# Kernel tuning notes

Hardware: AMD Instinct MI355X
Metric: run time of the kernel (lower is better)

## Reference

```python
import jax, jax.numpy as jnp
import numpy as np

N, D, O = 8192, 1024, 1024

def setup_inputs() -> dict:
    key = jax.random.key(0)
    ks = jax.random.split(key, 6)
    s = 1.0 / np.sqrt(D)
    x = jax.random.normal(ks[0], (N, D), dtype=jnp.float32)
    adj = jax.random.randint(ks[1], (N, N), 0, 2, dtype=jnp.int32)
    Wf = jax.random.normal(ks[2], (D, D), dtype=jnp.float32) * s
    Wg = jax.random.normal(ks[3], (D, D), dtype=jnp.float32) * s
    W = jax.random.normal(ks[4], (D, O), dtype=jnp.float32) * s
    bf = jnp.zeros((D,), dtype=jnp.float32)
    bg = jnp.zeros((D,), dtype=jnp.float32)
    bW = jnp.zeros((O,), dtype=jnp.float32)
    return {"x": x, "adj": adj, "Wf": Wf, "bf": bf, "Wg": Wg, "bg": bg, "W": W, "bW": bW}

def reference(x, adj, Wf, bf, Wg, bg, W, bW):
    NEG = jnp.float32(-9e15)
    f = x @ Wf + bf                      # [N, D]
    g = x @ Wg + bg                      # [N, D]
    e = jax.nn.relu(f @ g.T)             # [N, N] scores
    scores = jnp.where(adj > 0, e, NEG)  # adjacency mask
    attention = jax.nn.softmax(scores, axis=1)
    # dropout is identity in eval mode (training=False)
    x_W = x @ W + bW                     # [N, O]
    return attention @ x_W               # concat=False -> no final relu
```

## Files before the change

### kernel.cpp

```cpp
#include <hip/hip_runtime.h>
#include <stdint.h>

#define NROWS 8192
#define KDIM  1024
#define CAP   512
#define NEGBIG (-9.0e15f)
#define EMIT_THR 16.0f
#define SURV_THR 13.5f
#define MAXS  128

typedef __attribute__((ext_vector_type(8))) __bf16 bf16x8;
typedef __attribute__((ext_vector_type(4))) float f32x4;
typedef __attribute__((ext_vector_type(4))) unsigned short us4;
typedef __attribute__((ext_vector_type(4))) int i32x4;
typedef unsigned short u16;

__device__ __forceinline__ u16 f2bf(float f) {
  unsigned u = __float_as_uint(f);
  u += 0x7fffu + ((u >> 16) & 1u);
  return (u16)(u >> 16);
}
__device__ __forceinline__ float bf2f(u16 h) {
  return __uint_as_float(((unsigned)h) << 16);
}

__device__ __forceinline__ void glds16(const void* g, const char* lds) {
  __builtin_amdgcn_global_load_lds(
      (const __attribute__((address_space(1))) unsigned int*)(uintptr_t)g,
      (__attribute__((address_space(3))) unsigned int*)(uintptr_t)lds, 16, 0, 0);
}

__device__ __forceinline__ f32x4 mfma16(bf16x8 a, bf16x8 b, f32x4 c) {
  return __builtin_amdgcn_mfma_f32_16x16x32_bf16(a, b, c, 0, 0, 0);
}

template<int NSPLIT, bool SPLITOUT>
__global__ __launch_bounds__(512, 1) void gemm_kernel(
    const u16* __restrict__ ah, const u16* __restrict__ al,
    const u16* __restrict__ bh, const u16* __restrict__ bl,
    const float* __restrict__ bias, u16* __restrict__ ch, u16* __restrict__ cl)
{
  extern __shared__ char smem[];
  constexpr int BUFS = (NSPLIT == 3) ? 65536 : 32768;
  constexpr int AHO = 0, ALO = 16384;
  constexpr int BHO = (NSPLIT == 3) ? 32768 : 16384;
  constexpr int BLO = 49152;
  constexpr int NT = KDIM / 64;

  const int tid = threadIdx.x, w = tid >> 6, lane = tid & 63;
  const int wr = w >> 2, wc = w & 3;
  const int bx = blockIdx.x, by = blockIdx.y;
  const int arow0 = bx * 128, bcol0 = by * 128;

  const int srow = w * 16 + (lane >> 3);
  const int scol = ((lane & 7) ^ (lane >> 3)) * 8;
  const size_t sgA = (size_t)(arow0 + srow) * KDIM + scol;
  const size_t sgB = (size_t)(bcol0 + srow) * KDIM + scol;
  const int ldsw = w * 2048;

  auto stg = [&](const u16* src, size_t sg, int kt, int ldsoff) {
    const u16* sp = src + sg + kt * 64;
    glds16(sp,            smem + ldsoff + ldsw);
    glds16(sp + 8 * KDIM, smem + ldsoff + ldsw + 1024);
  };

  const int fa = (wr * 64 + (lane & 15)) * 128;
  const int fb = (wc * 32 + (lane & 15)) * 128;
  const int kqx0 = (((lane >> 4)    ) ^ (lane & 7)) * 16;
  const int kqx1 = (((lane >> 4) + 4) ^ (lane & 7)) * 16;

  stg(ah, sgA, 0, AHO); stg(bh, sgB, 0, BHO);
  if constexpr (NSPLIT == 3) { stg(al, sgA, 0, ALO); stg(bl, sgB, 0, BLO); }
  else { stg(ah, sgA, 1, AHO + BUFS); stg(bh, sgB, 1, BHO + BUFS); }

  f32x4 acc[4][2];
  #pragma unroll
  for (int m = 0; m < 4; ++m) {
    acc[m][0] = f32x4{0.f, 0.f, 0.f, 0.f};
    acc[m][1] = f32x4{0.f, 0.f, 0.f, 0.f};
  }

  for (int t = 0; t < NT; ++t) {
    const int bo  = (t & 1) * BUFS;
    const int bo2 = ((t + 1) & 1) * BUFS;

    if (NSPLIT == 1 && t == NT - 1) asm volatile("s_waitcnt vmcnt(0)" ::: "memory");
    else                            asm volatile("s_waitcnt vmcnt(4)" ::: "memory");
    __builtin_amdgcn_s_barrier();
    __builtin_amdgcn_sched_barrier(0);

    if (NSPLIT == 3 && t + 1 < NT) {
      stg(ah, sgA, t + 1, AHO + bo2);
      stg(bh, sgB, t + 1, BHO + bo2);
    }

    bf16x8 a0[4][2], b0[2][2];
    #pragma unroll
    for (int m = 0; m < 4; ++m) {
      a0[m][0] = *(const bf16x8*)(smem + AHO + bo + fa + m * 2048 + kqx0);
      a0[m][1] = *(const bf16x8*)(smem + AHO + bo + fa + m * 2048 + kqx1);
    }
    #pragma unroll
    for (int n = 0; n < 2; ++n) {
      b0[n][0] = *(const bf16x8*)(smem + BHO + bo + fb + n * 2048 + kqx0);
      b0[n][1] = *(const bf16x8*)(smem + BHO + bo + fb + n * 2048 + kqx1);
    }
    __builtin_amdgcn_s_setprio(1);
    #pragma unroll
    for (int kq = 0; kq < 2; ++kq)
      #pragma unroll
      for (int m = 0; m < 4; ++m)
        #pragma unroll
        for (int n = 0; n < 2; ++n)
          acc[m][n] = mfma16(a0[m][kq], b0[n][kq], acc[m][n]);
    __builtin_amdgcn_s_setprio(0);
    asm volatile("s_waitcnt lgkmcnt(0)" ::: "memory");

    if constexpr (NSPLIT == 3) {
      if (t + 1 < NT) asm volatile("s_waitcnt vmcnt(4)" ::: "memory");
      else            asm volatile("s_waitcnt vmcnt(0)" ::: "memory");
      __builtin_amdgcn_s_barrier();
      __builtin_amdgcn_sched_barrier(0);

      if (t + 1 < NT) {
        stg(al, sgA, t + 1, ALO + bo2);
        stg(bl, sgB, t + 1, BLO + bo2);
      }
      bf16x8 a1[4][2], b1[2][2];
      #pragma unroll
      for (int m = 0; m < 4; ++m) {
        a1[m][0] = *(const bf16x8*)(smem + ALO + bo + fa + m * 2048 + kqx0);
        a1[m][1] = *(const bf16x8*)(smem + ALO + bo + fa + m * 2048 + kqx1);
      }
      #pragma unroll
      for (int n = 0; n < 2; ++n) {
        b1[n][0] = *(const bf16x8*)(smem + BLO + bo + fb + n * 2048 + kqx0);
        b1[n][1] = *(const bf16x8*)(smem + BLO + bo + fb + n * 2048 + kqx1);
      }
      __builtin_amdgcn_s_setprio(1);
      #pragma unroll
      for (int kq = 0; kq < 2; ++kq)
        #pragma unroll
        for (int m = 0; m < 4; ++m)
          #pragma unroll
          for (int n = 0; n < 2; ++n)
            acc[m][n] = mfma16(a1[m][kq], b0[n][kq], acc[m][n]);
      #pragma unroll
      for (int kq = 0; kq < 2; ++kq)
        #pragma unroll
        for (int m = 0; m < 4; ++m)
          #pragma unroll
          for (int n = 0; n < 2; ++n)
            acc[m][n] = mfma16(a0[m][kq], b1[n][kq], acc[m][n]);
      __builtin_amdgcn_s_setprio(0);
      asm volatile("s_waitcnt lgkmcnt(0)" ::: "memory");
    } else {
      __builtin_amdgcn_s_barrier();
      if (t + 2 < NT) {
        stg(ah, sgA, t + 2, AHO + bo);
        stg(bh, sgB, t + 2, BHO + bo);
      }
    }
  }

  const int l15 = lane & 15, g4 = (lane >> 4) << 2;
  const int colb = bcol0 + wc * 32 + l15;
  const float bi0 = bias[colb], bi1 = bias[colb + 16];
  #pragma unroll
  for (int m = 0; m < 4; ++m) {
    #pragma unroll
    for (int j = 0; j < 4; ++j) {
      const int row = arow0 + wr * 64 + m * 16 + g4 + j;
      float v0 = acc[m][0][j] + bi0, v1 = acc[m][1][j] + bi1;
      u16 h0 = f2bf(v0), h1 = f2bf(v1);
      ch[(size_t)row * KDIM + colb] = h0;
      ch[(size_t)row * KDIM + colb + 16] = h1;
      if constexpr (SPLITOUT) {
        cl[(size_t)row * KDIM + colb] = f2bf(v0 - bf2f(h0));
        cl[(size_t)row * KDIM + colb + 16] = f2bf(v1 - bf2f(h1));
      }
    }
  }
}

__global__ __launch_bounds__(512, 2) void scores_kernel(
    const u16* __restrict__ fh, const u16* __restrict__ gh,
    const uint32_t* __restrict__ adjb, uint32_t* __restrict__ cand,
    int* __restrict__ cnts, int* rowmax)
{
  extern __shared__ char smem[];
  constexpr int NT = 64;

  const int tid = threadIdx.x, w = tid >> 6, lane = tid & 63;
  const int wr = w >> 2, wc = w & 3;
  const int l15 = lane & 15, g4 = (lane >> 4) << 2;

  const int xcd = blockIdx.x & 7, idx = blockIdx.x >> 3;
  const int bx  = xcd * 4 + (idx & 3);
  const int sub = idx >> 2;
  const int arow0 = bx * 256;

  const int srow = tid >> 3;
  const int skq  = (tid & 7) ^ (srow & 7);
  const int sdw  = w * 1024;

  auto stageA = [&](int T, int half) {
    char* d = smem + (T & 1) * 65536 + half * 16384 + sdw;
    const u16* s = fh + (size_t)(arow0 + half * 128 + srow) * KDIM
                      + (T & 15) * 64 + skq * 8;
    glds16(s, d);
    glds16(s + (size_t)64 * KDIM, d + 8192);
  };
  auto stageB = [&](int T, int half) {
    char* d = smem + (T & 1) * 65536 + 32768 + half * 16384 + sdw;
    const u16* s = gh + (size_t)((sub + 8 * (T >> 4)) * 256 + half * 128 + srow) * KDIM
                      + (T & 15) * 64 + skq * 8;
    glds16(s, d);
    glds16(s + (size_t)64 * KDIM, d + 8192);
  };

  const int kxa = ((lane >> 4) ^ (l15 & 7)) * 16;
  const int kxb = (((lane >> 4) + 4) ^ (l15 & 7)) * 16;
  const int abase = wr * 16384 + l15 * 128;
  const int bbase = 32768 + (wc >> 1) * 16384 + ((wc & 1) * 64 + l15) * 128;

  f32x4 acc[8][4];
  #pragma unroll
  for (int m = 0; m < 8; ++m)
    #pragma unroll
    for (int n = 0; n < 4; ++n) acc[m][n] = f32x4{0.f, 0.f, 0.f, 0.f};

  const unsigned long long lmask = (1ull << lane) - 1ull;
  const unsigned long long gm = 0xFFFFull << (lane & 48);

  stageA(0, 0); stageA(0, 1); stageB(0, 0); stageB(0, 1);
  stageA(1, 0); stageA(1, 1); stageB(1, 0); stageB(1, 1);
  asm volatile("s_waitcnt vmcnt(8)" ::: "memory");
  __builtin_amdgcn_s_barrier();

  bf16x8 a[8][2], b[4][2];

  for (int T = 0; T < NT; ++T) {
    const char* sb = smem + (T & 1) * 65536;

    #pragma unroll
    for (int m = 0; m < 4; ++m) {
      a[m][0] = *(const bf16x8*)(sb + abase + m * 2048 + kxa);
      a[m][1] = *(const bf16x8*)(sb + abase + m * 2048 + kxb);
    }
    #pragma unroll
    for (int n = 0; n < 2; ++n) {
      b[n][0] = *(const bf16x8*)(sb + bbase + n * 2048 + kxa);
      b[n][1] = *(const bf16x8*)(sb + bbase + n * 2048 + kxb);
    }
    __builtin_amdgcn_s_barrier();
    __builtin_amdgcn_s_setprio(1);
    #pragma unroll
    for (int kq = 0; kq < 2; ++kq)
      #pragma unroll
      for (int m = 0; m < 4; ++m)
        #pragma unroll
        for (int n = 0; n < 2; ++n)
          acc[m][n] = mfma16(a[m][kq], b[n][kq], acc[m][n]);
    __builtin_amdgcn_s_setprio(0);
    __builtin_amdgcn_s_barrier();

    #pragma unroll
    for (int m = 4; m < 8; ++m) {
      a[m][0] = *(const bf16x8*)(sb + abase + m * 2048 + kxa);
      a[m][1] = *(const bf16x8*)(sb + abase + m * 2048 + kxb);
    }
    __builtin_amdgcn_s_barrier();
    __builtin_amdgcn_s_setprio(1);
    #pragma unroll
    for (int kq = 0; kq < 2; ++kq)
      #pragma unroll
      for (int m = 4; m < 8; ++m)
        #pragma unroll
        for (int n = 0; n < 2; ++n)
          acc[m][n] = mfma16(a[m][kq], b[n][kq], acc[m][n]);
    __builtin_amdgcn_s_setprio(0);
    asm volatile("s_waitcnt lgkmcnt(0)" ::: "memory");
    __builtin_amdgcn_s_barrier();

    #pragma unroll
    for (int n = 2; n < 4; ++n) {
      b[n][0] = *(const bf16x8*)(sb + bbase + n * 2048 + kxa);
      b[n][1] = *(const bf16x8*)(sb + bbase + n * 2048 + kxb);
    }
    if (T + 2 < NT) { stageA(T + 2, 0); stageA(T + 2, 1); }
    __builtin_amdgcn_s_barrier();
    __builtin_amdgcn_s_setprio(1);
    #pragma unroll
    for (int kq = 0; kq < 2; ++kq)
      #pragma unroll
      for (int m = 0; m < 4; ++m)
        #pragma unroll
        for (int n = 2; n < 4; ++n)
          acc[m][n] = mfma16(a[m][kq], b[n][kq], acc[m][n]);
    __builtin_amdgcn_s_setprio(0);
    asm volatile("s_waitcnt lgkmcnt(0)" ::: "memory");
    __builtin_amdgcn_s_barrier();

    if (T + 2 < NT) {
      stageB(T + 2, 0); stageB(T + 2, 1);
      asm volatile("s_waitcnt vmcnt(8)" ::: "memory");
    } else {
      asm volatile("s_waitcnt vmcnt(0)" ::: "memory");
    }
    __builtin_amdgcn_s_barrier();
    __builtin_amdgcn_s_setprio(1);
    #pragma unroll
    for (int kq = 0; kq < 2; ++kq)
      #pragma unroll
      for (int m = 4; m < 8; ++m)
        #pragma unroll
        for (int n = 2; n < 4; ++n)
          acc[m][n] = mfma16(a[m][kq], b[n][kq], acc[m][n]);
    __builtin_amdgcn_s_setprio(0);
    __builtin_amdgcn_s_barrier();

    if ((T & 15) == 15) {
      const int it = T >> 4;
      const int bcol0 = (sub + 8 * it) * 256;
      const int keyb = bcol0 + wc * 64 + l15;
      #pragma unroll
      for (int mc = 0; mc < 4; ++mc) {
        uint32_t A0[2][4], A1[2][4]; float RX[2][4]; int ROW[2][4];
        #pragma unroll
        for (int mm = 0; mm < 2; ++mm)
          #pragma unroll
          for (int j = 0; j < 4; ++j) {
            const int m = mc * 2 + mm;
            const int row = arow0 + wr * 128 + m * 16 + g4 + j;
            ROW[mm][j] = row;
            const uint32_t* ap = adjb + (size_t)row * (NROWS / 32) + (bcol0 >> 5) + wc * 2;
            A0[mm][j] = ap[0];
            A1[mm][j] = ap[1];
            RX[mm][j] = __int_as_float(rowmax[row]);
          }
        float SV[2][4][4]; float TH[2][4]; int BS[2][4];
        #pragma unroll
        for (int mm = 0; mm < 2; ++mm)
          #pragma unroll
          for (int j = 0; j < 4; ++j) {
            const int m = mc * 2 + mm;
            float rm = NEGBIG;
            #pragma unroll
            for (int n = 0; n < 4; ++n) {
              float v = fmaxf(acc[m][n][j], 0.f);
              uint32_t bit = ((n < 2 ? A0[mm][j] : A1[mm][j]) >> ((n & 1) * 16 + l15)) & 1u;
              float s = bit ? v : NEGBIG;
              SV[mm][j][n] = s;
              rm = fmaxf(rm, s);
            }
            rm = fmaxf(rm, __shfl_xor(rm, 1));
            rm = fmaxf(rm, __shfl_xor(rm, 2));
            rm = fmaxf(rm, __shfl_xor(rm, 4));
            rm = fmaxf(rm, __shfl_xor(rm, 8));
            const float mr = fmaxf(rm, RX[mm][j]);
            if (l15 == 0 && rm > RX[mm][j])
              atomicMax(rowmax + ROW[mm][j], __float_as_int(rm));
            TH[mm][j] = mr - EMIT_THR;
            int tot = 0;
            #pragma unroll
            for (int n = 0; n < 4; ++n)
              tot += __popcll(__ballot(SV[mm][j][n] > TH[mm][j]) & gm);
            BS[mm][j] = 0;
            if (l15 == 0 && tot > 0)
              BS[mm][j] = atomicAdd(cnts + ROW[mm][j], tot);
          }
        #pragma unroll
        for (int mm = 0; mm < 2; ++mm)
          #pragma unroll
          for (int j = 0; j < 4; ++j) {
            int base = __shfl(BS[mm][j], lane & 48);
            int pref = 0;
            #pragma unroll
            for (int n = 0; n < 4; ++n) {
              unsigned long long mk = __ballot(SV[mm][j][n] > TH[mm][j]);
              const int p = base + pref + __popcll(mk & gm & lmask);
              if ((SV[mm][j][n] > TH[mm][j]) && p < CAP)
                cand[(size_t)ROW[mm][j] * CAP + p] =
                    ((uint32_t)f2bf(SV[mm][j][n]) << 16) | (uint32_t)(keyb + n * 16);
              pref += __popcll(mk & gm);
            }
          }
      }
      #pragma unroll
      for (int m = 0; m < 8; ++m)
        #pragma unroll
        for (int n = 0; n < 4; ++n) acc[m][n] = f32x4{0.f, 0.f, 0.f, 0.f};
    }
  }
}

__global__ __launch_bounds__(256) void adjpack_kernel(
    const int* __restrict__ adj, uint32_t* __restrict__ adjb)
{
  size_t w = (size_t)blockIdx.x * 256 + threadIdx.x;
  const int* src = adj + (w << 5);
  uint32_t m = 0;
  #pragma unroll
  for (int j = 0; j < 8; ++j) {
    i32x4 v = *(const i32x4*)(src + j * 4);
    m |= (v[0] > 0 ? 1u : 0u) << (j * 4)
       | (v[1] > 0 ? 1u : 0u) << (j * 4 + 1)
       | (v[2] > 0 ? 1u : 0u) << (j * 4 + 2)
       | (v[3] > 0 ? 1u : 0u) << (j * 4 + 3);
  }
  adjb[w] = m;
}

__global__ __launch_bounds__(256) void finalize_kernel(
    const uint32_t* __restrict__ cand, const int* __restrict__ cnts,
    const u16* __restrict__ fh, const u16* __restrict__ fl,
    const u16* __restrict__ gh, const u16* __restrict__ gl,
    const u16* __restrict__ vh, float* __restrict__ out)
{
  const int row = blockIdx.x, tid = threadIdx.x, wv = tid >> 6, lane = tid & 63;
  __shared__ float sS[CAP];
  __shared__ int sK[CAP];
  __shared__ float sF[KDIM];
  __shared__ float sEx[MAXS];
  __shared__ int sKs[MAXS];
  __shared__ float red[4];
  __shared__ int nsig;
  int cnt = cnts[row]; cnt = cnt < CAP ? cnt : CAP;
  const int col = tid * 4;
  if (cnt <= 0) {
    f32x4 z = {0.f, 0.f, 0.f, 0.f};
    *(f32x4*)(out + (size_t)row * KDIM + col) = z;
    return;
  }
  if (tid == 0) nsig = 0;
  {
    us4 h = *(const us4*)(fh + (size_t)row * KDIM + col);
    us4 l = *(const us4*)(fl + (size_t)row * KDIM + col);
    #pragma unroll
    for (int j = 0; j < 4; ++j) sF[col + j] = bf2f(h[j]) + bf2f(l[j]);
  }
  for (int i = tid; i < cnt; i += 256) {
    uint32_t pk = cand[(size_t)row * CAP + i];
    sS[i] = bf2f((u16)(pk >> 16));
    sK[i] = (int)(pk & 0xFFFFu);
  }
  __syncthreads();
  float lm = NEGBIG;
  for (int i = tid; i < cnt; i += 256) lm = fmaxf(lm, sS[i]);
  #pragma unroll
  for (int d = 1; d < 64; d <<= 1) lm = fmaxf(lm, __shfl_xor(lm, d));
  if ((tid & 63) == 0) red[tid >> 6] = lm;
  __syncthreads();
  const float am = fmaxf(fmaxf(red[0], red[1]), fmaxf(red[2], red[3]));
  __syncthreads();
  for (int i = tid; i < cnt; i += 256) {
    if (sS[i] > am - SURV_THR) {
      int p = atomicAdd(&nsig, 1);
      if (p < MAXS) { sKs[p] = sK[i]; sS[i] = NEGBIG; }
    }
  }
  __syncthreads();
  const int ns = nsig < MAXS ? nsig : MAXS;
  for (int si = wv; si < ns; si += 4) {
    const int key = sKs[si];
    const u16* grh = gh + (size_t)key * KDIM + lane * 16;
    const u16* grl = gl + (size_t)key * KDIM + lane * 16;
    float d = 0.f;
    #pragma unroll
    for (int u = 0; u < 4; ++u) {
      us4 h = *(const us4*)(grh + u * 4);
      us4 l = *(const us4*)(grl + u * 4);
      #pragma unroll
      for (int j = 0; j < 4; ++j)
        d += (bf2f(h[j]) + bf2f(l[j])) * sF[lane * 16 + u * 4 + j];
    }
    #pragma unroll
    for (int dd = 1; dd < 64; dd <<= 1) d += __shfl_xor(d, dd);
    if (lane == 0) sEx[si] = fmaxf(d, 0.f);
  }
  __syncthreads();
  float em = NEGBIG;
  for (int i = tid; i < ns; i += 256) em = fmaxf(em, sEx[i]);
  #pragma unroll
  for (int d = 1; d < 64; d <<= 1) em = fmaxf(em, __shfl_xor(em, d));
  if ((tid & 63) == 0) red[tid >> 6] = em;
  __syncthreads();
  const float m = fmaxf(fmaxf(red[0], red[1]), fmaxf(red[2], red[3]));
  __syncthreads();
  float ls = 0.f;
  for (int i = tid; i < cnt; i += 256) {
    float s = sS[i];
    if (s > NEGBIG * 0.5f) ls += __expf(s - m);
  }
  for (int i = tid; i < ns; i += 256) ls += __expf(sEx[i] - m);
  #pragma unroll
  for (int d = 1; d < 64; d <<= 1) ls += __shfl_xor(ls, d);
  if ((tid & 63) == 0) red[tid >> 6] = ls;
  __syncthreads();
  const float inv = 1.f / (red[0] + red[1] + red[2] + red[3]);
  float a0 = 0.f, a1 = 0.f, a2 = 0.f, a3 = 0.f;
  const u16* vbase = vh + col;
  for (int i = 0; i < ns; ++i) {
    const float wt = __expf(sEx[i] - m) * inv;
    us4 vv = *(const us4*)(vbase + (size_t)sKs[i] * KDIM);
    a0 += wt * bf2f(vv[0]); a1 += wt * bf2f(vv[1]);
    a2 += wt * bf2f(vv[2]); a3 += wt * bf2f(vv[3]);
  }
  f32x4 o = {a0, a1, a2, a3};
  *(f32x4*)(out + (size_t)row * KDIM + col) = o;
}

__global__ __launch_bounds__(256) void wsplit_kernel(
    const float* __restrict__ W, u16* __restrict__ th, u16* __restrict__ tl)
{
  __shared__ float tile[32][33];
  const int bx = blockIdx.x, by = blockIdx.y;
  const int tx = threadIdx.x & 31, ty = threadIdx.x >> 5;
  #pragma unroll
  for (int i = 0; i < 4; ++i) {
    int ky = ty + i * 8;
    tile[ky][tx] = W[(size_t)(by * 32 + ky) * KDIM + bx * 32 + tx];
  }
  __syncthreads();
  #pragma unroll
  for (int i = 0; i < 4; ++i) {
    int ny = ty + i * 8;
    float v = tile[tx][ny];
    u16 h = f2bf(v);
    th[(size_t)(bx * 32 + ny) * KDIM + by * 32 + tx] = h;
    tl[(size_t)(bx * 32 + ny) * KDIM + by * 32 + tx] = f2bf(v - bf2f(h));
  }
}

__global__ __launch_bounds__(256) void xsplit_kernel(
    const float* __restrict__ x, u16* __restrict__ xh, u16* __restrict__ xl)
{
  size_t i = ((size_t)blockIdx.x * 256 + threadIdx.x) * 4;
  f32x4 v = *(const f32x4*)(x + i);
  us4 h, l;
  #pragma unroll
  for (int j = 0; j < 4; ++j) {
    h[j] = f2bf(v[j]);
    l[j] = f2bf(v[j] - bf2f(h[j]));
  }
  *(us4*)(xh + i) = h;
  *(us4*)(xl + i) = l;
}

__global__ void ws_report(float* out, size_t n, float v) {
  for (size_t i = (size_t)blockIdx.x * blockDim.x + threadIdx.x; i < n;
       i += (size_t)gridDim.x * blockDim.x) out[i] = v;
}

extern "C" void kernel_launch(void* const* d_in, const int* in_sizes, int n_in,
                              void* d_out, int out_size, void* d_ws, size_t ws_size,
                              hipStream_t stream) {
  (void)in_sizes; (void)n_in;
  const float* x   = (const float*)d_in[0];
  const int*   adj = (const int*)d_in[1];
  const float* Wf  = (const float*)d_in[2];
  const float* bf_ = (const float*)d_in[3];
  const float* Wg  = (const float*)d_in[4];
  const float* bg_ = (const float*)d_in[5];
  const float* W   = (const float*)d_in[6];
  const float* bW_ = (const float*)d_in[7];

  char* p = (char*)d_ws;
  const size_t ND2 = (size_t)NROWS * KDIM * 2;
  const size_t W2  = (size_t)KDIM * KDIM * 2;
  u16* xh = (u16*)p;  p += ND2;
  u16* xl = (u16*)p;  p += ND2;
  u16* fh = (u16*)p;  p += ND2;
  u16* fl = (u16*)p;  p += ND2;
  u16* gh = (u16*)p;  p += ND2;
  u16* gl = (u16*)p;  p += ND2;
  u16* vh = (u16*)p;  p += ND2;
  u16* wfh = (u16*)p; p += W2;
  u16* wfl = (u16*)p; p += W2;
  u16* wgh = (u16*)p; p += W2;
  u16* wgl = (u16*)p; p += W2;
  u16* wh  = (u16*)p; p += W2;
  u16* wl  = (u16*)p; p += W2;
  uint32_t* cand = (uint32_t*)p; p += (size_t)NROWS * CAP * 4;
  int* cnts   = (int*)p; p += (size_t)NROWS * 4;
  int* rowmax = (int*)p; p += (size_t)NROWS * 4;
  const size_t need = (size_t)(p - (char*)d_ws);
  if (ws_size < need) {
    ws_report<<<256, 256, 0, stream>>>((float*)d_out, (size_t)out_size, (float)ws_size);
    return;
  }
  uint32_t* adjb = (uint32_t*)xl;

  auto kf = gemm_kernel<3, true>;
  auto kv = gemm_kernel<1, false>;
  hipFuncSetAttribute((const void*)kf, hipFuncAttributeMaxDynamicSharedMemorySize, 131072);
  hipFuncSetAttribute((const void*)kv, hipFuncAttributeMaxDynamicSharedMemorySize, 65536);
  hipFuncSetAttribute((const void*)scores_kernel, hipFuncAttributeMaxDynamicSharedMemorySize, 131072);

  hipMemsetAsync(cnts, 0, (size_t)NROWS * 8, stream);
  wsplit_kernel<<<dim3(32, 32), 256, 0, stream>>>(Wf, wfh, wfl);
  wsplit_kernel<<<dim3(32, 32), 256, 0, stream>>>(Wg, wgh, wgl);
  wsplit_kernel<<<dim3(32, 32), 256, 0, stream>>>(W, wh, wl);
  xsplit_kernel<<<(NROWS * KDIM) / (256 * 4), 256, 0, stream>>>(x, xh, xl);

  kf<<<dim3(64, 8), 512, 131072, stream>>>(xh, xl, wfh, wfl, bf_, fh, fl);
  kf<<<dim3(64, 8), 512, 131072, stream>>>(xh, xl, wgh, wgl, bg_, gh, gl);
  kv<<<dim3(64, 8), 512, 65536, stream>>>(xh, xl, wh, wl, bW_, vh, nullptr);
  adjpack_kernel<<<(NROWS * (NROWS / 32)) / 256, 256, 0, stream>>>(adj, adjb);
  scores_kernel<<<dim3(256), 512, 131072, stream>>>(fh, gh, adjb, cand, cnts, rowmax);
  finalize_kernel<<<NROWS, 256, 0, stream>>>(cand, cnts, fh, fl, gh, gl, vh,
                                             (float*)d_out);
}
```

Before: 558.3 us.

## Quantize f and g to fp8 for the candidate-screening scores GEMM

Adds a quant_kernel that converts the bf16 f and g activations to fp8 e4m3 and reorders each row's k-chunks to match the MFMA operand layout. The scores_kernel now stages the fp8 data and uses the 16x16x32 fp8 MFMA, which halves its LDS and global traffic and the number of K tiles. The emit threshold is raised to absorb the larger fp8 error in the screening pass; exact values are still recomputed in finalize from the split-bf16 data. The risks are extra candidates filling the per-row cap, and two extra kernel launches plus an extra pass over f and g.

```diff
diff --git a/kernel.cpp b/kernel.cpp
--- a/kernel.cpp
+++ b/kernel.cpp
@@ -5,7 +5,7 @@
 #define KDIM  1024
 #define CAP   512
 #define NEGBIG (-9.0e15f)
-#define EMIT_THR 16.0f
+#define EMIT_THR 20.0f
 #define SURV_THR 13.5f
 #define MAXS  128
 
@@ -13,7 +13,10 @@
 typedef __attribute__((ext_vector_type(4))) float f32x4;
 typedef __attribute__((ext_vector_type(4))) unsigned short us4;
 typedef __attribute__((ext_vector_type(4))) int i32x4;
+typedef __attribute__((ext_vector_type(2))) long i64x2;
+typedef __attribute__((ext_vector_type(16))) unsigned char u8x16;
 typedef unsigned short u16;
+typedef unsigned char u8;
 
 __device__ __forceinline__ u16 f2bf(float f) {
   unsigned u = __float_as_uint(f);
@@ -24,6 +27,28 @@
   return __uint_as_float(((unsigned)h) << 16);
 }
 
+__device__ __forceinline__ u8 f2fp8(float f) {
+  uint32_t u = __float_as_uint(f);
+  uint32_t s = (u >> 24) & 0x80u;
+  int e = (int)((u >> 23) & 0xffu) - 127;
+  uint32_t m = u & 0x7fffffu;
+  if (e > 8 || (e == 8 && m > 0x600000u)) return (u8)(s | 0x7eu);
+  if (e >= -6) {
+    uint32_t mant = m >> 20;
+    uint32_t rem = m & 0xfffffu;
+    if (rem > 0x80000u || (rem == 0x80000u && (mant & 1u))) mant++;
+    uint32_t ee = (uint32_t)(e + 7);
+    if (mant == 8u) { mant = 0u; ee++; }
+    if (ee >= 16u) return (u8)(s | 0x7eu);
+    return (u8)(s | (ee << 3) | mant);
+  }
+  if (e < -10) return (u8)s;
+  float af = fabsf(f);
+  int q = (int)(af * 512.0f + 0.5f);
+  if (q > 8) q = 8;
+  return (u8)(s | (uint32_t)q);
+}
+
 __device__ __forceinline__ void glds16(const void* g, const char* lds) {
   __builtin_amdgcn_global_load_lds(
       (const __attribute__((address_space(1))) unsigned int*)(uintptr_t)g,
@@ -32,6 +57,9 @@
 
 __device__ __forceinline__ f32x4 mfma16(bf16x8 a, bf16x8 b, f32x4 c) {
   return __builtin_amdgcn_mfma_f32_16x16x32_bf16(a, b, c, 0, 0, 0);
+}
+__device__ __forceinline__ f32x4 mfma8(long a, long b, f32x4 c) {
+  return __builtin_amdgcn_mfma_f32_16x16x32_fp8_fp8(a, b, c, 0, 0, 0);
 }
 
 template<int NSPLIT, bool SPLITOUT>
@@ -183,46 +211,67 @@
   }
 }
 
+__global__ __launch_bounds__(256) void quant_kernel(
+    const u16* __restrict__ src, u8* __restrict__ dst)
+{
+  const int id = blockIdx.x * 256 + threadIdx.x;
+  const int row = id >> 6, mtc = id & 63;
+  const int mt = mtc >> 3, c = mtc & 7;
+  const int k0 = mt * 128 + (c >> 2) * 64 + (c & 3) * 8;
+  const u16* s0 = src + (size_t)row * KDIM + k0;
+  u8x16 o;
+  #pragma unroll
+  for (int j = 0; j < 8; ++j) o[j] = f2fp8(bf2f(s0[j]));
+  #pragma unroll
+  for (int j = 0; j < 8; ++j) o[8 + j] = f2fp8(bf2f(s0[32 + j]));
+  *(u8x16*)(dst + (size_t)id * 16) = o;
+}
+
 __global__ __launch_bounds__(512, 2) void scores_kernel(
-    const u16* __restrict__ fh, const u16* __restrict__ gh,
+    const u8* __restrict__ fq, const u8* __restrict__ gq,
     const uint32_t* __restrict__ adjb, uint32_t* __restrict__ cand,
     int* __restrict__ cnts, int* rowmax)
 {
   extern __shared__ char smem[];
-  constexpr int NT = 64;
+  constexpr int NT = 32;
 
   const int tid = threadIdx.x, w = tid >> 6, lane = tid & 63;
   const int wr = w >> 2, wc = w & 3;
-  const int l15 = lane & 15, g4 = (lane >> 4) << 2;
+  const int l15 = lane & 15, g4 = (lane >> 4) << 2, hi4 = lane >> 4;
 
   const int xcd = blockIdx.x & 7, idx = blockIdx.x >> 3;
   const int bx  = xcd * 4 + (idx & 3);
   const int sub = idx >> 2;
   const int arow0 = bx * 256;
 
-  const int srow = tid >> 3;
-  const int skq  = (tid & 7) ^ (srow & 7);
-  const int sdw  = w * 1024;
-
-  auto stageA = [&](int T, int half) {
-    char* d = smem + (T & 1) * 65536 + half * 16384 + sdw;
-    const u16* s = fh + (size_t)(arow0 + half * 128 + srow) * KDIM
-                      + (T & 15) * 64 + skq * 8;
-    glds16(s, d);
-    glds16(s + (size_t)64 * KDIM, d + 8192);
+  const int sdw = w * 4096;
+
+  auto stageA = [&](int T) {
+    char* dbase = smem + (T & 1) * 65536 + sdw;
+    #pragma unroll
+    for (int i = 0; i < 4; ++i) {
+      const int d = (w * 4 + i) * 64 + lane;
+      const int row = d >> 3, cl = (d & 7) ^ (row & 7);
+      glds16(fq + (size_t)(arow0 + row) * KDIM + (T & 7) * 128 + cl * 16,
+             dbase + i * 1024);
+    }
   };
-  auto stageB = [&](int T, int half) {
-    char* d = smem + (T & 1) * 65536 + 32768 + half * 16384 + sdw;
-    const u16* s = gh + (size_t)((sub + 8 * (T >> 4)) * 256 + half * 128 + srow) * KDIM
-                      + (T & 15) * 64 + skq * 8;
-    glds16(s, d);
-    glds16(s + (size_t)64 * KDIM, d + 8192);
+  auto stageB = [&](int T) {
+    char* dbase = smem + (T & 1) * 65536 + 32768 + sdw;
+    const size_t kb = (size_t)(sub + 8 * (T >> 3)) * 256;
+    #pragma unroll
+    for (int i = 0; i < 4; ++i) {
+      const int d = (w * 4 + i) * 64 + lane;
+      const int row = d >> 3, cl = (d & 7) ^ (row & 7);
+      glds16(gq + (kb + row) * KDIM + (T & 7) * 128 + cl * 16,
+             dbase + i * 1024);
+    }
   };
 
-  const int kxa = ((lane >> 4) ^ (l15 & 7)) * 16;
-  const int kxb = (((lane >> 4) + 4) ^ (l15 & 7)) * 16;
+  const int kxp0 = ((hi4    ) ^ (l15 & 7)) * 16;
+  const int kxp1 = ((hi4 + 4) ^ (l15 & 7)) * 16;
   const int abase = wr * 16384 + l15 * 128;
-  const int bbase = 32768 + (wc >> 1) * 16384 + ((wc & 1) * 64 + l15) * 128;
+  const int bbase = 32768 + (wc * 64 + l15) * 128;
 
   f32x4 acc[8][4];
   #pragma unroll
@@ -233,77 +282,83 @@
   const unsigned long long lmask = (1ull << lane) - 1ull;
   const unsigned long long gm = 0xFFFFull << (lane & 48);
 
-  stageA(0, 0); stageA(0, 1); stageB(0, 0); stageB(0, 1);
-  stageA(1, 0); stageA(1, 1); stageB(1, 0); stageB(1, 1);
+  stageA(0); stageB(0);
+  stageA(1); stageB(1);
   asm volatile("s_waitcnt vmcnt(8)" ::: "memory");
   __builtin_amdgcn_s_barrier();
 
-  bf16x8 a[8][2], b[4][2];
+  i64x2 a[8][2], b[4][2];
 
   for (int T = 0; T < NT; ++T) {
     const char* sb = smem + (T & 1) * 65536;
 
     #pragma unroll
     for (int m = 0; m < 4; ++m) {
-      a[m][0] = *(const bf16x8*)(sb + abase + m * 2048 + kxa);
-      a[m][1] = *(const bf16x8*)(sb + abase + m * 2048 + kxb);
+      a[m][0] = *(const i64x2*)(sb + abase + m * 2048 + kxp0);
+      a[m][1] = *(const i64x2*)(sb + abase + m * 2048 + kxp1);
     }
     #pragma unroll
     for (int n = 0; n < 2; ++n) {
-      b[n][0] = *(const bf16x8*)(sb + bbase + n * 2048 + kxa);
-      b[n][1] = *(const bf16x8*)(sb + bbase + n * 2048 + kxb);
+      b[n][0] = *(const i64x2*)(sb + bbase + n * 2048 + kxp0);
+      b[n][1] = *(const i64x2*)(sb + bbase + n * 2048 + kxp1);
     }
     __builtin_amdgcn_s_barrier();
     __builtin_amdgcn_s_setprio(1);
     #pragma unroll
-    for (int kq = 0; kq < 2; ++kq)
-      #pragma unroll
-      for (int m = 0; m < 4; ++m)
-        #pragma unroll
-        for (int n = 0; n < 2; ++n)
-          acc[m][n] = mfma16(a[m][kq], b[n][kq], acc[m][n]);
+    for (int kp = 0; kp < 2; ++kp)
+      #pragma unroll
+      for (int kh = 0; kh < 2; ++kh)
+        #pragma unroll
+        for (int m = 0; m < 4; ++m)
+          #pragma unroll
+          for (int n = 0; n < 2; ++n)
+            acc[m][n] = mfma8(a[m][kp][kh], b[n][kp][kh], acc[m][n]);
     __builtin_amdgcn_s_setprio(0);
     __builtin_amdgcn_s_barrier();
 
     #pragma unroll
     for (int m = 4; m < 8; ++m) {
-      a[m][0] = *(const bf16x8*)(sb + abase + m * 2048 + kxa);
-      a[m][1] = *(const bf16x8*)(sb + abase + m * 2048 + kxb);
+      a[m][0] = *(const i64x2*)(sb + abase + m * 2048 + kxp0);
+      a[m][1] = *(const i64x2*)(sb + abase + m * 2048 + kxp1);
     }
     __builtin_amdgcn_s_barrier();
     __builtin_amdgcn_s_setprio(1);
     #pragma unroll
-    for (int kq = 0; kq < 2; ++kq)
-      #pragma unroll
-      for (int m = 4; m < 8; ++m)
-        #pragma unroll
-        for (int n = 0; n < 2; ++n)
-          acc[m][n] = mfma16(a[m][kq], b[n][kq], acc[m][n]);
+    for (int kp = 0; kp < 2; ++kp)
+      #pragma unroll
+      for (int kh = 0; kh < 2; ++kh)
+        #pragma unroll
+        for (int m = 4; m < 8; ++m)
+          #pragma unroll
+          for (int n = 0; n < 2; ++n)
+            acc[m][n] = mfma8(a[m][kp][kh], b[n][kp][kh], acc[m][n]);
     __builtin_amdgcn_s_setprio(0);
     asm volatile("s_waitcnt lgkmcnt(0)" ::: "memory");
     __builtin_amdgcn_s_barrier();
 
     #pragma unroll
     for (int n = 2; n < 4; ++n) {
-      b[n][0] = *(const bf16x8*)(sb + bbase + n * 2048 + kxa);
-      b[n][1] = *(const bf16x8*)(sb + bbase + n * 2048 + kxb);
-    }
-    if (T + 2 < NT) { stageA(T + 2, 0); stageA(T + 2, 1); }
+      b[n][0] = *(const i64x2*)(sb + bbase + n * 2048 + kxp0);
+      b[n][1] = *(const i64x2*)(sb + bbase + n * 2048 + kxp1);
+    }
+    if (T + 2 < NT) stageA(T + 2);
     __builtin_amdgcn_s_barrier();
     __builtin_amdgcn_s_setprio(1);
     #pragma unroll
-    for (int kq = 0; kq < 2; ++kq)
-      #pragma unroll
-      for (int m = 0; m < 4; ++m)
-        #pragma unroll
-        for (int n = 2; n < 4; ++n)
-          acc[m][n] = mfma16(a[m][kq], b[n][kq], acc[m][n]);
+    for (int kp = 0; kp < 2; ++kp)
+      #pragma unroll
+      for (int kh = 0; kh < 2; ++kh)
+        #pragma unroll
+        for (int m = 0; m < 4; ++m)
+          #pragma unroll
+          for (int n = 2; n < 4; ++n)
+            acc[m][n] = mfma8(a[m][kp][kh], b[n][kp][kh], acc[m][n]);
     __builtin_amdgcn_s_setprio(0);
     asm volatile("s_waitcnt lgkmcnt(0)" ::: "memory");
     __builtin_amdgcn_s_barrier();
 
     if (T + 2 < NT) {
-      stageB(T + 2, 0); stageB(T + 2, 1);
+      stageB(T + 2);
       asm volatile("s_waitcnt vmcnt(8)" ::: "memory");
     } else {
       asm volatile("s_waitcnt vmcnt(0)" ::: "memory");
@@ -311,17 +366,19 @@
     __builtin_amdgcn_s_barrier();
     __builtin_amdgcn_s_setprio(1);
     #pragma unroll
-    for (int kq = 0; kq < 2; ++kq)
-      #pragma unroll
-      for (int m = 4; m < 8; ++m)
-        #pragma unroll
-        for (int n = 2; n < 4; ++n)
-          acc[m][n] = mfma16(a[m][kq], b[n][kq], acc[m][n]);
+    for (int kp = 0; kp < 2; ++kp)
+      #pragma unroll
+      for (int kh = 0; kh < 2; ++kh)
+        #pragma unroll
+        for (int m = 4; m < 8; ++m)
+          #pragma unroll
+          for (int n = 2; n < 4; ++n)
+            acc[m][n] = mfma8(a[m][kp][kh], b[n][kp][kh], acc[m][n]);
     __builtin_amdgcn_s_setprio(0);
     __builtin_amdgcn_s_barrier();
 
-    if ((T & 15) == 15) {
-      const int it = T >> 4;
+    if ((T & 7) == 7) {
+      const int it = T >> 3;
       const int bcol0 = (sub + 8 * it) * 256;
       const int keyb = bcol0 + wc * 64 + l15;
       #pragma unroll
@@ -568,6 +625,7 @@
 
   char* p = (char*)d_ws;
   const size_t ND2 = (size_t)NROWS * KDIM * 2;
+  const size_t ND1 = (size_t)NROWS * KDIM;
   const size_t W2  = (size_t)KDIM * KDIM * 2;
   u16* xh = (u16*)p;  p += ND2;
   u16* xl = (u16*)p;  p += ND2;
@@ -582,6 +640,8 @@
   u16* wgl = (u16*)p; p += W2;
   u16* wh  = (u16*)p; p += W2;
   u16* wl  = (u16*)p; p += W2;
+  u8* fq = (u8*)p; p += ND1;
+  u8* gq = (u8*)p; p += ND1;
   uint32_t* cand = (uint32_t*)p; p += (size_t)NROWS * CAP * 4;
   int* cnts   = (int*)p; p += (size_t)NROWS * 4;
   int* rowmax = (int*)p; p += (size_t)NROWS * 4;
@@ -607,8 +667,10 @@
   kf<<<dim3(64, 8), 512, 131072, stream>>>(xh, xl, wfh, wfl, bf_, fh, fl);
   kf<<<dim3(64, 8), 512, 131072, stream>>>(xh, xl, wgh, wgl, bg_, gh, gl);
   kv<<<dim3(64, 8), 512, 65536, stream>>>(xh, xl, wh, wl, bW_, vh, nullptr);
+  quant_kernel<<<(NROWS * 64) / 256, 256, 0, stream>>>(fh, fq);
+  quant_kernel<<<(NROWS * 64) / 256, 256, 0, stream>>>(gh, gq);
   adjpack_kernel<<<(NROWS * (NROWS / 32)) / 256, 256, 0, stream>>>(adj, adjb);
-  scores_kernel<<<dim3(256), 512, 131072, stream>>>(fh, gh, adjb, cand, cnts, rowmax);
+  scores_kernel<<<dim3(256), 512, 131072, stream>>>(fq, gq, adjb, cand, cnts, rowmax);
   finalize_kernel<<<NROWS, 256, 0, stream>>>(cand, cnts, fh, fl, gh, gl, vh,
                                              (float*)d_out);
 }
```

Result: slower. 583.6 us (+4.5%).
